# Optimization experiments

Hardware: AMD Instinct MI355X
Metric: run time of the kernel (lower is better)

## Reference

```python
import jax, jax.numpy as jnp
import numpy as np

B, S, D = 16, 2048, 128
NEG = -1000000000.0


def setup_inputs() -> dict:
    key = jax.random.key(0)
    kq, kk, kv = jax.random.split(key, 3)
    q = jax.random.normal(kq, (B, S, D), dtype=jnp.float32)
    k = jax.random.normal(kk, (B, S, D), dtype=jnp.float32)
    v = jax.random.normal(kv, (B, S, D), dtype=jnp.float32)
    # causal mask: True entries are masked out (filled with -1e9)
    mask = jnp.broadcast_to(
        jnp.triu(jnp.ones((S, S), dtype=bool), k=1)[None, :, :], (B, S, S)
    )
    return {"q": q, "k": k, "v": v, "mask": mask}


def reference(q, k, v, mask):
    # attn = q @ k^T / sqrt(d_k), masked_fill, softmax over keys, attn @ v
    scale = jnp.sqrt(jnp.asarray(D, dtype=q.dtype))
    attn = jnp.einsum("bqd,bkd->bqk", q, k) / scale
    attn = jnp.where(mask, jnp.asarray(NEG, dtype=attn.dtype), attn)
    attn = jax.nn.softmax(attn, axis=2)
    out = jnp.einsum("bqk,bkd->bqd", attn, v)
    return (out, attn)
```

## Files before the change

### kernel.cpp

```cpp
#include <hip/hip_runtime.h>

#define B_ 16
#define S_ 2048
#define D_ 128

typedef __attribute__((ext_vector_type(8))) short bf16x8;
typedef __attribute__((ext_vector_type(4))) float f32x4;
typedef __attribute__((ext_vector_type(16))) float f32x16;
typedef __attribute__((ext_vector_type(2))) unsigned int u32x2;
typedef __attribute__((ext_vector_type(4))) unsigned int u32x4;

__device__ __forceinline__ unsigned short f2bf(float f) {
    unsigned int u = __builtin_bit_cast(unsigned int, f);
    u += 0x7fff + ((u >> 16) & 1);
    return (unsigned short)(u >> 16);
}

__device__ __forceinline__ void gload16(const void* g, void* l) {
    __builtin_amdgcn_global_load_lds(
        (const __attribute__((address_space(1))) void*)g,
        (__attribute__((address_space(3))) void*)l, 16, 0, 0);
}

#define WAITV(n) asm volatile("s_waitcnt vmcnt(" #n ")" ::: "memory")

__global__ __launch_bounds__(256, 4)
void conv_kv(const float* __restrict__ kg, const float* __restrict__ vg,
             char* __restrict__ kws, char* __restrict__ vws)
{
    __shared__ float lt[64 * 132];
    const int bid = blockIdx.x;
    if (bid < 512) {
        const float* src = kg + ((long)bid << 13);
        char* dst = kws + ((long)bid << 14);
#pragma unroll
        for (int it = 0; it < 4; ++it) {
            const int c = threadIdx.x + it * 256;
            const int r = c >> 4, j = c & 15;
            f32x4 a = *(const f32x4*)(src + r * 128 + j * 8);
            f32x4 cc = *(const f32x4*)(src + r * 128 + j * 8 + 4);
            u32x4 p;
            p[0] = (unsigned)f2bf(a[0]) | ((unsigned)f2bf(a[1]) << 16);
            p[1] = (unsigned)f2bf(a[2]) | ((unsigned)f2bf(a[3]) << 16);
            p[2] = (unsigned)f2bf(cc[0]) | ((unsigned)f2bf(cc[1]) << 16);
            p[3] = (unsigned)f2bf(cc[2]) | ((unsigned)f2bf(cc[3]) << 16);
            *(u32x4*)(dst + r * 256 + ((j ^ (r & 7)) << 4)) = p;
        }
    } else {
        const int vb = bid - 512;
        const float* src = vg + ((long)vb << 13);
        char* dst = vws + ((long)vb << 14);
#pragma unroll
        for (int it = 0; it < 8; ++it) {
            const int c = threadIdx.x + it * 256;
            const int r = c >> 5, q = c & 31;
            *(f32x4*)(lt + r * 132 + q * 4) = *(const f32x4*)(src + r * 128 + q * 4);
        }
        __syncthreads();
#pragma unroll
        for (int it = 0; it < 4; ++it) {
            const int c = threadIdx.x + it * 256;
            const int d = c >> 3, jc = c & 7;
            unsigned short e[8];
#pragma unroll
            for (int ee = 0; ee < 8; ++ee) e[ee] = f2bf(lt[(jc * 8 + ee) * 132 + d]);
            u32x4 p;
            p[0] = (unsigned)e[0] | ((unsigned)e[1] << 16);
            p[1] = (unsigned)e[2] | ((unsigned)e[3] << 16);
            p[2] = (unsigned)e[4] | ((unsigned)e[5] << 16);
            p[3] = (unsigned)e[6] | ((unsigned)e[7] << 16);
            *(u32x4*)(dst + d * 128 + ((jc ^ (d & 7)) << 4)) = p;
        }
    }
}

__device__ __forceinline__ int qtile_of(int b, int t) {
    const int f = (t & 1) ? (t >> 1) : (31 - (t >> 1));
    return (b & 8) ? (31 - f) : f;
}

__global__ __launch_bounds__(256, 4)
void sumexp(const float* __restrict__ qg, const char* __restrict__ kws,
            float* __restrict__ lg, float* __restrict__ attng)
{
    __shared__ char kT[2][16384];

    const int tid = threadIdx.x, lane = tid & 63, w = tid >> 6;
    const int l15 = lane & 15, l4 = lane >> 4;
    const int bid = blockIdx.x;
    const int b = bid >> 5;
    const int qt = qtile_of(b, bid & 31);
    const int q0 = qt * 64;
    const float scale = 0.088388347648318447f;

    bf16x8 qf[4];
    {
        const float* qrow = qg + ((long)b * S_ + q0 + w * 16 + l15) * D_;
#pragma unroll
        for (int kk = 0; kk < 4; ++kk) {
            const int d0 = kk * 32 + l4 * 8;
            f32x4 a = *(const f32x4*)(qrow + d0);
            f32x4 c = *(const f32x4*)(qrow + d0 + 4);
            bf16x8 tt;
            tt[0] = (short)f2bf(a[0]); tt[1] = (short)f2bf(a[1]);
            tt[2] = (short)f2bf(a[2]); tt[3] = (short)f2bf(a[3]);
            tt[4] = (short)f2bf(c[0]); tt[5] = (short)f2bf(c[1]);
            tt[6] = (short)f2bf(c[2]); tt[7] = (short)f2bf(c[3]);
            qf[kk] = tt;
        }
    }
    WAITV(0);

    float sum[4] = {0.f, 0.f, 0.f, 0.f};
    const char* kb0 = kws + ((long)(b * 32) << 14);

#pragma unroll
    for (int it = 0; it < 4; ++it)
        gload16(kb0 + (w * 4 + it) * 1024 + lane * 16, &kT[0][(w * 4 + it) * 1024]);

    int buf = 0;
    for (int kt = 0; kt <= qt; ++kt) {
        const bool pf = (kt < qt);
        if (pf) {
            const char* kn = kb0 + ((long)(kt + 1) << 14);
#pragma unroll
            for (int it = 0; it < 4; ++it)
                gload16(kn + (w * 4 + it) * 1024 + lane * 16, &kT[buf ^ 1][(w * 4 + it) * 1024]);
            WAITV(4);
        } else {
            WAITV(0);
        }
        __builtin_amdgcn_s_barrier();
        __builtin_amdgcn_sched_barrier(0);

        f32x4 acc[4];
        __builtin_amdgcn_s_setprio(1);
#pragma unroll
        for (int n = 0; n < 4; ++n) {
            f32x4 a = {0.f, 0.f, 0.f, 0.f};
            const int krow = n * 16 + l15;
            const int rb = krow * 256;
            const int swz = (krow & 7) << 4;
#pragma unroll
            for (int kk = 0; kk < 4; ++kk) {
                bf16x8 bf = *(const bf16x8*)(&kT[buf][rb + ((l4 * 16 + kk * 64) ^ swz)]);
                a = __builtin_amdgcn_mfma_f32_16x16x32_bf16(qf[kk], bf, a, 0, 0, 0);
            }
            acc[n] = a;
        }
        __builtin_amdgcn_s_setprio(0);

        const bool diag = (kt == qt);
#pragma unroll
        for (int n = 0; n < 4; ++n)
#pragma unroll
            for (int r = 0; r < 4; ++r) {
                if (!(diag && (n * 16 + l15 > w * 16 + l4 * 4 + r)))
                    sum[r] += __expf(acc[n][r] * scale);
            }
        __builtin_amdgcn_sched_barrier(0);
        __builtin_amdgcn_s_barrier();
        buf ^= 1;
    }

#pragma unroll
    for (int off = 1; off < 16; off <<= 1)
#pragma unroll
        for (int r = 0; r < 4; ++r)
            sum[r] += __shfl_xor(sum[r], off, 64);
    if (l15 == 0) {
#pragma unroll
        for (int r = 0; r < 4; ++r)
            lg[(long)b * S_ + q0 + w * 16 + l4 * 4 + r] = 1.f / sum[r];
    }

    float* attn_base = attng + ((long)b * S_ + q0) * S_;
    const int col0 = (qt + 1) * 64;
    if (col0 < S_) {
        const int nch = (S_ - col0) >> 2;
        const f32x4 z = {0.f, 0.f, 0.f, 0.f};
        for (int row = w; row < 64; row += 4) {
            float* rbase = attn_base + (long)row * S_ + col0;
            for (int c = lane; c < nch; c += 64)
                *(f32x4*)(rbase + c * 4) = z;
        }
    }
}

__global__ __launch_bounds__(256, 2)
void attn_pv(const float* __restrict__ qg, const char* __restrict__ kws,
             const char* __restrict__ vws, const float* __restrict__ lg,
             float* __restrict__ outg, float* __restrict__ attng)
{
    __shared__ char lds[65536];

    const int tid = threadIdx.x, lane = tid & 63, w = tid >> 6;
    const int wq = w >> 1, wk = w & 1;
    const int l31 = lane & 31, hi = lane >> 5;
    const int bid = blockIdx.x;
    const int b = bid >> 5;
    const int qti = qtile_of(b, bid & 31);
    const int q0 = qti * 64;
    const int nt = qti + 1;
    const float scale = 0.088388347648318447f;
    const int qrow = q0 + wq * 32 + l31;

    bf16x8 qf[8];
    {
        const float* qr = qg + ((long)b * S_ + qrow) * D_;
#pragma unroll
        for (int km = 0; km < 8; ++km) {
            const int d0 = km * 16 + hi * 8;
            f32x4 a = *(const f32x4*)(qr + d0);
            f32x4 c = *(const f32x4*)(qr + d0 + 4);
            bf16x8 t;
            t[0] = (short)f2bf(a[0]); t[1] = (short)f2bf(a[1]);
            t[2] = (short)f2bf(a[2]); t[3] = (short)f2bf(a[3]);
            t[4] = (short)f2bf(c[0]); t[5] = (short)f2bf(c[1]);
            t[6] = (short)f2bf(c[2]); t[7] = (short)f2bf(c[3]);
            qf[km] = t;
        }
    }
    const float invl_l = lg[(long)b * S_ + qrow];
    WAITV(0);

    f32x16 oacc[4];
#pragma unroll
    for (int dt = 0; dt < 4; ++dt)
#pragma unroll
        for (int i = 0; i < 16; ++i) oacc[dt][i] = 0.f;

    const char* kb0 = kws + ((long)(b * 32) << 14);
    const char* vb0 = vws + ((long)(b * 32) << 14);

#pragma unroll
    for (int it = 0; it < 4; ++it)
        gload16(kb0 + it * 4096 + tid * 16, lds + it * 4096 + tid * 16);
#pragma unroll
    for (int it = 0; it < 4; ++it)
        gload16(vb0 + it * 4096 + tid * 16, lds + 32768 + it * 4096 + tid * 16);

    const int krow = wk * 32 + l31;
    const int krb = krow * 256;
    const int ksw = krow & 7;

    int buf = 0;
    for (int kt = 0; kt < nt; ++kt) {
        const bool pf = (kt + 1 < nt);
        if (pf) {
            const char* kn = kb0 + ((long)(kt + 1) << 14);
            const char* vn = vb0 + ((long)(kt + 1) << 14);
            const int db = (buf ^ 1) * 16384;
#pragma unroll
            for (int it = 0; it < 4; ++it)
                gload16(kn + it * 4096 + tid * 16, lds + db + it * 4096 + tid * 16);
#pragma unroll
            for (int it = 0; it < 4; ++it)
                gload16(vn + it * 4096 + tid * 16, lds + 32768 + db + it * 4096 + tid * 16);
        }
        if (kt == 0) { if (pf) { WAITV(8); } else { WAITV(0); } }
        else         { if (pf) { WAITV(12); } else { WAITV(4); } }
        __builtin_amdgcn_s_barrier();
        __builtin_amdgcn_sched_barrier(0);

        const char* kbuf = lds + buf * 16384;
        const char* vbuf = lds + 32768 + buf * 16384;

        f32x16 acc;
#pragma unroll
        for (int i = 0; i < 16; ++i) acc[i] = 0.f;
        __builtin_amdgcn_s_setprio(1);
#pragma unroll
        for (int km = 0; km < 8; ++km) {
            bf16x8 kf = *(const bf16x8*)(kbuf + krb + (((km * 2 + hi) ^ ksw) << 4));
            acc = __builtin_amdgcn_mfma_f32_32x32x16_bf16(kf, qf[km], acc, 0, 0, 0);
        }
        __builtin_amdgcn_s_setprio(0);

        const int kbase = kt * 64 + wk * 32;
        float p[16];
#pragma unroll
        for (int r = 0; r < 16; ++r) {
            const int kl = (r & 3) + 8 * (r >> 2) + 4 * hi;
            p[r] = (kbase + kl > qrow) ? 0.f : __expf(acc[r] * scale);
        }
        unsigned W[8], PW[8];
#pragma unroll
        for (int i = 0; i < 8; ++i)
            W[i] = (unsigned)f2bf(p[2 * i]) | ((unsigned)f2bf(p[2 * i + 1]) << 16);
#pragma unroll
        for (int i = 0; i < 8; ++i)
            PW[i] = (unsigned)__shfl_xor((int)W[i], 32, 64);

        bf16x8 pa[2];
        float* arow = attng + ((long)b * S_ + qrow) * S_ + kbase;
#pragma unroll
        for (int kc = 0; kc < 2; ++kc) {
            u32x4 fr;
            fr[0] = hi ? PW[kc * 4 + 2] : W[kc * 4 + 0];
            fr[1] = hi ? PW[kc * 4 + 3] : W[kc * 4 + 1];
            fr[2] = hi ? W[kc * 4 + 2] : PW[kc * 4 + 0];
            fr[3] = hi ? W[kc * 4 + 3] : PW[kc * 4 + 1];
            pa[kc] = __builtin_bit_cast(bf16x8, fr);
            f32x4 s0, s1;
            s0[0] = __builtin_bit_cast(float, fr[0] << 16) * invl_l;
            s0[1] = __builtin_bit_cast(float, fr[0] & 0xffff0000u) * invl_l;
            s0[2] = __builtin_bit_cast(float, fr[1] << 16) * invl_l;
            s0[3] = __builtin_bit_cast(float, fr[1] & 0xffff0000u) * invl_l;
            s1[0] = __builtin_bit_cast(float, fr[2] << 16) * invl_l;
            s1[1] = __builtin_bit_cast(float, fr[2] & 0xffff0000u) * invl_l;
            s1[2] = __builtin_bit_cast(float, fr[3] << 16) * invl_l;
            s1[3] = __builtin_bit_cast(float, fr[3] & 0xffff0000u) * invl_l;
            *(f32x4*)(arow + kc * 16 + hi * 8) = s0;
            *(f32x4*)(arow + kc * 16 + hi * 8 + 4) = s1;
        }

        __builtin_amdgcn_s_setprio(1);
#pragma unroll
        for (int dt = 0; dt < 4; ++dt) {
            const int d = dt * 32 + l31;
            const int rowb = d * 128;
            const int sw = (d & 7) << 4;
#pragma unroll
            for (int kc = 0; kc < 2; ++kc) {
                const int jc = wk * 4 + kc * 2 + hi;
                bf16x8 vf = *(const bf16x8*)(vbuf + rowb + ((jc << 4) ^ sw));
                oacc[dt] = __builtin_amdgcn_mfma_f32_32x32x16_bf16(pa[kc], vf, oacc[dt], 0, 0, 0);
            }
        }
        __builtin_amdgcn_s_setprio(0);
        __builtin_amdgcn_sched_barrier(0);
        __builtin_amdgcn_s_barrier();
        buf ^= 1;
    }

    __syncthreads();
    float* red = (float*)lds;
    if (wk) {
#pragma unroll
        for (int dt = 0; dt < 4; ++dt)
#pragma unroll
            for (int r = 0; r < 16; ++r) {
                const int qr = (r & 3) + 8 * (r >> 2) + 4 * hi;
                red[wq * 4096 + qr * 128 + dt * 32 + l31] = oacc[dt][r];
            }
    }
    __syncthreads();
    if (!wk) {
        float iv[16];
#pragma unroll
        for (int r = 0; r < 16; ++r) {
            const int qr = (r & 3) + 8 * (r >> 2) + 4 * hi;
            iv[r] = __shfl(invl_l, qr, 64);
        }
        float* ob = outg + ((long)b * S_ + q0 + wq * 32) * D_;
#pragma unroll
        for (int dt = 0; dt < 4; ++dt)
#pragma unroll
            for (int r = 0; r < 16; ++r) {
                const int qr = (r & 3) + 8 * (r >> 2) + 4 * hi;
                ob[(long)qr * D_ + dt * 32 + l31] =
                    (oacc[dt][r] + red[wq * 4096 + qr * 128 + dt * 32 + l31]) * iv[r];
            }
    }
}

__global__ __launch_bounds__(256, 2)
void attn_fallback(const float* __restrict__ qg, const float* __restrict__ kg,
                   const float* __restrict__ vg,
                   float* __restrict__ outg, float* __restrict__ attng)
{
    __shared__ unsigned short kT[64 * 128];
    __shared__ unsigned short vT[128 * 64];
    __shared__ unsigned short pT[4][16 * 64];
    const int tid = threadIdx.x, lane = tid & 63, w = tid >> 6;
    const int l15 = lane & 15, l4 = lane >> 4;
    const int bid = blockIdx.x;
    const int b = bid >> 5, qt = 31 - (bid & 31), q0 = qt * 64;
    const float scale = 0.088388347648318447f;
    bf16x8 qf[4];
    {
        const float* qrow = qg + ((long)b * S_ + q0 + w * 16 + l15) * D_;
#pragma unroll
        for (int kk = 0; kk < 4; ++kk) {
            const int d0 = kk * 32 + l4 * 8;
            f32x4 a = *(const f32x4*)(qrow + d0);
            f32x4 c = *(const f32x4*)(qrow + d0 + 4);
            bf16x8 t;
            t[0] = (short)f2bf(a[0]); t[1] = (short)f2bf(a[1]);
            t[2] = (short)f2bf(a[2]); t[3] = (short)f2bf(a[3]);
            t[4] = (short)f2bf(c[0]); t[5] = (short)f2bf(c[1]);
            t[6] = (short)f2bf(c[2]); t[7] = (short)f2bf(c[3]);
            qf[kk] = t;
        }
    }
    float m[4], l[4];
#pragma unroll
    for (int r = 0; r < 4; ++r) { m[r] = -1e30f; l[r] = 0.f; }
    for (int kt = 0; kt <= qt; ++kt) {
        __syncthreads();
        {
            const float* kbase = kg + ((long)b * S_ + kt * 64) * D_;
#pragma unroll
            for (int it = 0; it < 8; ++it) {
                const int c = tid + it * 256, row = c >> 5, dc = c & 31;
                f32x4 a = *(const f32x4*)(kbase + row * D_ + dc * 4);
                u32x2 p;
                p[0] = (unsigned)f2bf(a[0]) | ((unsigned)f2bf(a[1]) << 16);
                p[1] = (unsigned)f2bf(a[2]) | ((unsigned)f2bf(a[3]) << 16);
                *(u32x2*)((char*)kT + row * 256 + ((dc * 8) ^ ((row & 7) << 4))) = p;
            }
        }
        __syncthreads();
        f32x4 acc[4];
#pragma unroll
        for (int n = 0; n < 4; ++n) {
            f32x4 a = {0.f, 0.f, 0.f, 0.f};
            const int krow = n * 16 + l15, rb = krow * 256, swz = (krow & 7) << 4;
#pragma unroll
            for (int kk = 0; kk < 4; ++kk) {
                bf16x8 bf = *(const bf16x8*)((const char*)kT + rb + ((l4 * 16 + kk * 64) ^ swz));
                a = __builtin_amdgcn_mfma_f32_16x16x32_bf16(qf[kk], bf, a, 0, 0, 0);
            }
            acc[n] = a;
        }
        const bool diag = (kt == qt);
        float tm[4] = {-3e38f, -3e38f, -3e38f, -3e38f};
#pragma unroll
        for (int n = 0; n < 4; ++n)
#pragma unroll
            for (int r = 0; r < 4; ++r) {
                float s = acc[n][r] * scale;
                if (diag && (n * 16 + l15 > w * 16 + l4 * 4 + r)) s = -3e38f;
                acc[n][r] = s; tm[r] = fmaxf(tm[r], s);
            }
#pragma unroll
        for (int off = 1; off < 16; off <<= 1)
#pragma unroll
            for (int r = 0; r < 4; ++r) tm[r] = fmaxf(tm[r], __shfl_xor(tm[r], off, 64));
        float sum[4], mn[4];
#pragma unroll
        for (int r = 0; r < 4; ++r) {
            mn[r] = fmaxf(m[r], tm[r]);
            float s0 = 0.f;
#pragma unroll
            for (int n = 0; n < 4; ++n) s0 += __expf(acc[n][r] - mn[r]);
            sum[r] = s0;
        }
#pragma unroll
        for (int off = 1; off < 16; off <<= 1)
#pragma unroll
            for (int r = 0; r < 4; ++r) sum[r] += __shfl_xor(sum[r], off, 64);
#pragma unroll
        for (int r = 0; r < 4; ++r) { l[r] = l[r] * __expf(m[r] - mn[r]) + sum[r]; m[r] = mn[r]; }
    }
    float invl[4];
#pragma unroll
    for (int r = 0; r < 4; ++r) invl[r] = 1.f / l[r];
    f32x4 oacc[8];
#pragma unroll
    for (int n = 0; n < 8; ++n) oacc[n] = (f32x4){0.f, 0.f, 0.f, 0.f};
    float* attn_base = attng + ((long)b * S_ + q0) * S_;
    for (int kt = 0; kt <= qt; ++kt) {
        __syncthreads();
        {
            const float* kbase = kg + ((long)b * S_ + kt * 64) * D_;
#pragma unroll
            for (int it = 0; it < 8; ++it) {
                const int c = tid + it * 256, row = c >> 5, dc = c & 31;
                f32x4 a = *(const f32x4*)(kbase + row * D_ + dc * 4);
                u32x2 p;
                p[0] = (unsigned)f2bf(a[0]) | ((unsigned)f2bf(a[1]) << 16);
                p[1] = (unsigned)f2bf(a[2]) | ((unsigned)f2bf(a[3]) << 16);
                *(u32x2*)((char*)kT + row * 256 + ((dc * 8) ^ ((row & 7) << 4))) = p;
            }
        }
        {
            const float* vbase = vg + ((long)b * S_ + kt * 64) * D_;
#pragma unroll
            for (int it = 0; it < 8; ++it) {
                const int c = tid + it * 256, kr = c & 63, dq = c >> 6;
                f32x4 a = *(const f32x4*)(vbase + kr * D_ + dq * 4);
#pragma unroll
                for (int j = 0; j < 4; ++j) {
                    const int d = dq * 4 + j;
                    *(unsigned short*)((char*)vT + d * 128 + ((kr * 2) ^ ((d & 7) << 4))) = f2bf(a[j]);
                }
            }
        }
        __syncthreads();
        f32x4 acc[4];
#pragma unroll
        for (int n = 0; n < 4; ++n) {
            f32x4 a = {0.f, 0.f, 0.f, 0.f};
            const int krow = n * 16 + l15, rb = krow * 256, swz = (krow & 7) << 4;
#pragma unroll
            for (int kk = 0; kk < 4; ++kk) {
                bf16x8 bf = *(const bf16x8*)((const char*)kT + rb + ((l4 * 16 + kk * 64) ^ swz));
                a = __builtin_amdgcn_mfma_f32_16x16x32_bf16(qf[kk], bf, a, 0, 0, 0);
            }
            acc[n] = a;
        }
        const bool diag = (kt == qt);
#pragma unroll
        for (int n = 0; n < 4; ++n)
#pragma unroll
            for (int r = 0; r < 4; ++r) {
                float s = acc[n][r] * scale;
                if (diag && (n * 16 + l15 > w * 16 + l4 * 4 + r)) s = -3e38f;
                const float p = __expf(s - m[r]) * invl[r];
                attn_base[(long)(w * 16 + l4 * 4 + r) * S_ + kt * 64 + n * 16 + l15] = p;
                const int prow = l4 * 4 + r;
                *(unsigned short*)((char*)&pT[w][0] + prow * 128 + ((n * 32 + l15 * 2) ^ ((prow & 7) << 4))) = f2bf(p);
            }
        asm volatile("s_waitcnt lgkmcnt(0)" ::: "memory");
        __builtin_amdgcn_sched_barrier(0);
        bf16x8 pa[2];
#pragma unroll
        for (int kk = 0; kk < 2; ++kk)
            pa[kk] = *(const bf16x8*)((const char*)&pT[w][0] + l15 * 128 + ((l4 * 16 + kk * 64) ^ ((l15 & 7) << 4)));
#pragma unroll
        for (int n = 0; n < 8; ++n) {
            const int vrow = n * 16 + l15, rb = vrow * 128, swz = (vrow & 7) << 4;
#pragma unroll
            for (int kk = 0; kk < 2; ++kk) {
                bf16x8 bv = *(const bf16x8*)((const char*)vT + rb + ((l4 * 16 + kk * 64) ^ swz));
                oacc[n] = __builtin_amdgcn_mfma_f32_16x16x32_bf16(pa[kk], bv, oacc[n], 0, 0, 0);
            }
        }
    }
    {
        float* obase = outg + ((long)b * S_ + q0 + w * 16) * D_;
#pragma unroll
        for (int n = 0; n < 8; ++n)
#pragma unroll
            for (int r = 0; r < 4; ++r)
                obase[(long)(l4 * 4 + r) * D_ + n * 16 + l15] = oacc[n][r];
    }
    {
        const int col0 = (qt + 1) * 64;
        if (col0 < S_) {
            const int nch = (S_ - col0) >> 2;
            const f32x4 z = {0.f, 0.f, 0.f, 0.f};
            for (int row = w; row < 64; row += 4) {
                float* rbase = attn_base + (long)row * S_ + col0;
                for (int c = lane; c < nch; c += 64)
                    *(f32x4*)(rbase + c * 4) = z;
            }
        }
    }
}

extern "C" void kernel_launch(void* const* d_in, const int* in_sizes, int n_in,
                              void* d_out, int out_size, void* d_ws, size_t ws_size,
                              hipStream_t stream) {
    const float* q = (const float*)d_in[0];
    const float* k = (const float*)d_in[1];
    const float* v = (const float*)d_in[2];
    float* out  = (float*)d_out;
    float* attn = out + (long)B_ * S_ * D_;
    const size_t NEED = 131072 + 2u * 8388608u;
    if (ws_size >= NEED) {
        float* lg = (float*)d_ws;
        char* kws = (char*)d_ws + 131072;
        char* vws = kws + 8388608;
        conv_kv<<<dim3(1024), dim3(256), 0, stream>>>(k, v, kws, vws);
        sumexp<<<dim3(512), dim3(256), 0, stream>>>(q, kws, lg, attn);
        attn_pv<<<dim3(512), dim3(256), 0, stream>>>(q, kws, vws, lg, out, attn);
    } else {
        attn_fallback<<<dim3(512), dim3(256), 0, stream>>>(q, k, v, out, attn);
    }
}
```

Measured before the change: 120.3 us.

## Pre-layout K/V in MFMA fragment order and load directly to registers

The conversion kernel now writes bf16 K and V into a layout that matches the per-lane MFMA operand order, so sumexp and attn_pv read fragments straight from global memory into registers instead of staging through LDS with async copies and barriers. Work is reassigned per block as two 32-row query strips paired from opposite ends (strip u and 63-u) for causal load balance, with the two key halves split across waves and reduced through a small shared buffer. Register prefetch of the next K/V tile replaces LDS double buffering. This removes LDS traffic and barrier synchronisation but relies on L2 for reuse and raises register pressure.

After: 139.9 us. +16.3%, slower.

```diff
diff --git a/kernel.cpp b/kernel.cpp
--- a/kernel.cpp
+++ b/kernel.cpp
@@ -15,14 +15,6 @@
     u += 0x7fff + ((u >> 16) & 1);
     return (unsigned short)(u >> 16);
 }
-
-__device__ __forceinline__ void gload16(const void* g, void* l) {
-    __builtin_amdgcn_global_load_lds(
-        (const __attribute__((address_space(1))) void*)g,
-        (__attribute__((address_space(3))) void*)l, 16, 0, 0);
-}
-
-#define WAITV(n) asm volatile("s_waitcnt vmcnt(" #n ")" ::: "memory")
 
 __global__ __launch_bounds__(256, 4)
 void conv_kv(const float* __restrict__ kg, const float* __restrict__ vg,
@@ -44,7 +36,8 @@
             p[1] = (unsigned)f2bf(a[2]) | ((unsigned)f2bf(a[3]) << 16);
             p[2] = (unsigned)f2bf(cc[0]) | ((unsigned)f2bf(cc[1]) << 16);
             p[3] = (unsigned)f2bf(cc[2]) | ((unsigned)f2bf(cc[3]) << 16);
-            *(u32x4*)(dst + r * 256 + ((j ^ (r & 7)) << 4)) = p;
+            const int h = r >> 5, l31 = r & 31, km = j >> 1, hi = j & 1;
+            *(u32x4*)(dst + h * 8192 + km * 1024 + (hi * 32 + l31) * 16) = p;
         }
     } else {
         const int vb = bid - 512;
@@ -69,120 +62,92 @@
             p[1] = (unsigned)e[2] | ((unsigned)e[3] << 16);
             p[2] = (unsigned)e[4] | ((unsigned)e[5] << 16);
             p[3] = (unsigned)e[6] | ((unsigned)e[7] << 16);
-            *(u32x4*)(dst + d * 128 + ((jc ^ (d & 7)) << 4)) = p;
+            const int h = jc >> 2, kc = (jc >> 1) & 1, hi = jc & 1;
+            const int dt = d >> 5, l31 = d & 31;
+            *(u32x4*)(dst + h * 8192 + dt * 2048 + kc * 1024 + (hi * 32 + l31) * 16) = p;
         }
     }
 }
 
-__device__ __forceinline__ int qtile_of(int b, int t) {
-    const int f = (t & 1) ? (t >> 1) : (31 - (t >> 1));
-    return (b & 8) ? (31 - f) : f;
-}
 
 __global__ __launch_bounds__(256, 4)
 void sumexp(const float* __restrict__ qg, const char* __restrict__ kws,
             float* __restrict__ lg, float* __restrict__ attng)
 {
-    __shared__ char kT[2][16384];
-
+    __shared__ float redsum[2][2][32];
     const int tid = threadIdx.x, lane = tid & 63, w = tid >> 6;
-    const int l15 = lane & 15, l4 = lane >> 4;
+    const int l31 = lane & 31, hi = lane >> 5;
     const int bid = blockIdx.x;
-    const int b = bid >> 5;
-    const int qt = qtile_of(b, bid & 31);
-    const int q0 = qt * 64;
+    const int b = bid >> 5, u = bid & 31;
+    const int sidx = w >> 1, kh = w & 1;
+    const int strip = sidx ? u : (63 - u);
+    const int q0 = strip * 32;
+    const int qrow = q0 + l31;
+    const int nst = strip + 1;
     const float scale = 0.088388347648318447f;
 
-    bf16x8 qf[4];
+    bf16x8 qf[8];
     {
-        const float* qrow = qg + ((long)b * S_ + q0 + w * 16 + l15) * D_;
-#pragma unroll
-        for (int kk = 0; kk < 4; ++kk) {
-            const int d0 = kk * 32 + l4 * 8;
-            f32x4 a = *(const f32x4*)(qrow + d0);
-            f32x4 c = *(const f32x4*)(qrow + d0 + 4);
+        const float* qr = qg + ((long)b * S_ + qrow) * D_;
+#pragma unroll
+        for (int km = 0; km < 8; ++km) {
+            const int d0 = km * 16 + hi * 8;
+            f32x4 a = *(const f32x4*)(qr + d0);
+            f32x4 c = *(const f32x4*)(qr + d0 + 4);
             bf16x8 tt;
             tt[0] = (short)f2bf(a[0]); tt[1] = (short)f2bf(a[1]);
             tt[2] = (short)f2bf(a[2]); tt[3] = (short)f2bf(a[3]);
             tt[4] = (short)f2bf(c[0]); tt[5] = (short)f2bf(c[1]);
             tt[6] = (short)f2bf(c[2]); tt[7] = (short)f2bf(c[3]);
-            qf[kk] = tt;
-        }
-    }
-    WAITV(0);
-
-    float sum[4] = {0.f, 0.f, 0.f, 0.f};
+            qf[km] = tt;
+        }
+    }
+
     const char* kb0 = kws + ((long)(b * 32) << 14);
-
-#pragma unroll
-    for (int it = 0; it < 4; ++it)
-        gload16(kb0 + (w * 4 + it) * 1024 + lane * 16, &kT[0][(w * 4 + it) * 1024]);
-
-    int buf = 0;
-    for (int kt = 0; kt <= qt; ++kt) {
-        const bool pf = (kt < qt);
-        if (pf) {
-            const char* kn = kb0 + ((long)(kt + 1) << 14);
-#pragma unroll
-            for (int it = 0; it < 4; ++it)
-                gload16(kn + (w * 4 + it) * 1024 + lane * 16, &kT[buf ^ 1][(w * 4 + it) * 1024]);
-            WAITV(4);
-        } else {
-            WAITV(0);
-        }
-        __builtin_amdgcn_s_barrier();
-        __builtin_amdgcn_sched_barrier(0);
-
-        f32x4 acc[4];
-        __builtin_amdgcn_s_setprio(1);
-#pragma unroll
-        for (int n = 0; n < 4; ++n) {
-            f32x4 a = {0.f, 0.f, 0.f, 0.f};
-            const int krow = n * 16 + l15;
-            const int rb = krow * 256;
-            const int swz = (krow & 7) << 4;
-#pragma unroll
-            for (int kk = 0; kk < 4; ++kk) {
-                bf16x8 bf = *(const bf16x8*)(&kT[buf][rb + ((l4 * 16 + kk * 64) ^ swz)]);
-                a = __builtin_amdgcn_mfma_f32_16x16x32_bf16(qf[kk], bf, a, 0, 0, 0);
-            }
-            acc[n] = a;
-        }
-        __builtin_amdgcn_s_setprio(0);
-
-        const bool diag = (kt == qt);
-#pragma unroll
-        for (int n = 0; n < 4; ++n)
-#pragma unroll
-            for (int r = 0; r < 4; ++r) {
-                if (!(diag && (n * 16 + l15 > w * 16 + l4 * 4 + r)))
-                    sum[r] += __expf(acc[n][r] * scale);
-            }
-        __builtin_amdgcn_sched_barrier(0);
-        __builtin_amdgcn_s_barrier();
-        buf ^= 1;
-    }
-
-#pragma unroll
-    for (int off = 1; off < 16; off <<= 1)
-#pragma unroll
-        for (int r = 0; r < 4; ++r)
-            sum[r] += __shfl_xor(sum[r], off, 64);
-    if (l15 == 0) {
-#pragma unroll
-        for (int r = 0; r < 4; ++r)
-            lg[(long)b * S_ + q0 + w * 16 + l4 * 4 + r] = 1.f / sum[r];
-    }
-
-    float* attn_base = attng + ((long)b * S_ + q0) * S_;
-    const int col0 = (qt + 1) * 64;
+    float sum = 0.f;
+    if (kh < nst) {
+        bf16x8 kf[8];
+#pragma unroll
+        for (int km = 0; km < 8; ++km)
+            kf[km] = *(const bf16x8*)(kb0 + kh * 8192 + km * 1024 + lane * 16);
+        for (int j = kh; j < nst; j += 2) {
+            f32x16 acc;
+#pragma unroll
+            for (int i = 0; i < 16; ++i) acc[i] = 0.f;
+            __builtin_amdgcn_s_setprio(1);
+#pragma unroll
+            for (int km = 0; km < 8; ++km)
+                acc = __builtin_amdgcn_mfma_f32_32x32x16_bf16(kf[km], qf[km], acc, 0, 0, 0);
+            __builtin_amdgcn_s_setprio(0);
+            if (j + 2 < nst) {
+                const char* kn = kb0 + ((j + 2) >> 1) * 16384 + ((j + 2) & 1) * 8192;
+#pragma unroll
+                for (int km = 0; km < 8; ++km)
+                    kf[km] = *(const bf16x8*)(kn + km * 1024 + lane * 16);
+            }
+            const int kbase = j * 32;
+#pragma unroll
+            for (int r = 0; r < 16; ++r) {
+                const int kl = (r & 3) + 8 * (r >> 2) + 4 * hi;
+                if (kbase + kl <= qrow) sum += __expf(acc[r] * scale);
+            }
+        }
+    }
+    sum += __shfl_xor(sum, 32, 64);
+    redsum[sidx][kh][l31] = sum;
+    __syncthreads();
+    if (kh == 0 && !hi)
+        lg[(long)b * S_ + qrow] = 1.f / (sum + redsum[sidx][1][l31]);
+
+    const int col0 = ((strip >> 1) + 1) * 64;
     if (col0 < S_) {
         const int nch = (S_ - col0) >> 2;
         const f32x4 z = {0.f, 0.f, 0.f, 0.f};
-        for (int row = w; row < 64; row += 4) {
-            float* rbase = attn_base + (long)row * S_ + col0;
+        float* base = attng + ((long)b * S_ + q0 + kh * 16) * S_ + col0;
+        for (int row = 0; row < 16; ++row) {
+            float* rb = base + (long)row * S_;
             for (int c = lane; c < nch; c += 64)
-                *(f32x4*)(rbase + c * 4) = z;
+                *(f32x4*)(rb + c * 4) = z;
         }
     }
 }
@@ -192,18 +157,17 @@
              const char* __restrict__ vws, const float* __restrict__ lg,
              float* __restrict__ outg, float* __restrict__ attng)
 {
-    __shared__ char lds[65536];
-
+    __shared__ float red[2][32][128];
     const int tid = threadIdx.x, lane = tid & 63, w = tid >> 6;
-    const int wq = w >> 1, wk = w & 1;
     const int l31 = lane & 31, hi = lane >> 5;
     const int bid = blockIdx.x;
-    const int b = bid >> 5;
-    const int qti = qtile_of(b, bid & 31);
-    const int q0 = qti * 64;
-    const int nt = qti + 1;
+    const int b = bid >> 5, u = bid & 31;
+    const int sidx = w >> 1, kh = w & 1;
+    const int strip = sidx ? u : (63 - u);
+    const int q0 = strip * 32;
+    const int qrow = q0 + l31;
+    const int nst = (strip | 1) + 1;
     const float scale = 0.088388347648318447f;
-    const int qrow = q0 + wq * 32 + l31;
 
     bf16x8 qf[8];
     {
@@ -213,16 +177,15 @@
             const int d0 = km * 16 + hi * 8;
             f32x4 a = *(const f32x4*)(qr + d0);
             f32x4 c = *(const f32x4*)(qr + d0 + 4);
-            bf16x8 t;
-            t[0] = (short)f2bf(a[0]); t[1] = (short)f2bf(a[1]);
-            t[2] = (short)f2bf(a[2]); t[3] = (short)f2bf(a[3]);
-            t[4] = (short)f2bf(c[0]); t[5] = (short)f2bf(c[1]);
-            t[6] = (short)f2bf(c[2]); t[7] = (short)f2bf(c[3]);
-            qf[km] = t;
+            bf16x8 tt;
+            tt[0] = (short)f2bf(a[0]); tt[1] = (short)f2bf(a[1]);
+            tt[2] = (short)f2bf(a[2]); tt[3] = (short)f2bf(a[3]);
+            tt[4] = (short)f2bf(c[0]); tt[5] = (short)f2bf(c[1]);
+            tt[6] = (short)f2bf(c[2]); tt[7] = (short)f2bf(c[3]);
+            qf[km] = tt;
         }
     }
     const float invl_l = lg[(long)b * S_ + qrow];
-    WAITV(0);
 
     f32x16 oacc[4];
 #pragma unroll
@@ -232,68 +195,49 @@
 
     const char* kb0 = kws + ((long)(b * 32) << 14);
     const char* vb0 = vws + ((long)(b * 32) << 14);
-
-#pragma unroll
-    for (int it = 0; it < 4; ++it)
-        gload16(kb0 + it * 4096 + tid * 16, lds + it * 4096 + tid * 16);
-#pragma unroll
-    for (int it = 0; it < 4; ++it)
-        gload16(vb0 + it * 4096 + tid * 16, lds + 32768 + it * 4096 + tid * 16);
-
-    const int krow = wk * 32 + l31;
-    const int krb = krow * 256;
-    const int ksw = krow & 7;
-
-    int buf = 0;
-    for (int kt = 0; kt < nt; ++kt) {
-        const bool pf = (kt + 1 < nt);
-        if (pf) {
-            const char* kn = kb0 + ((long)(kt + 1) << 14);
-            const char* vn = vb0 + ((long)(kt + 1) << 14);
-            const int db = (buf ^ 1) * 16384;
-#pragma unroll
-            for (int it = 0; it < 4; ++it)
-                gload16(kn + it * 4096 + tid * 16, lds + db + it * 4096 + tid * 16);
-#pragma unroll
-            for (int it = 0; it < 4; ++it)
-                gload16(vn + it * 4096 + tid * 16, lds + 32768 + db + it * 4096 + tid * 16);
-        }
-        if (kt == 0) { if (pf) { WAITV(8); } else { WAITV(0); } }
-        else         { if (pf) { WAITV(12); } else { WAITV(4); } }
-        __builtin_amdgcn_s_barrier();
-        __builtin_amdgcn_sched_barrier(0);
-
-        const char* kbuf = lds + buf * 16384;
-        const char* vbuf = lds + 32768 + buf * 16384;
-
+    float* attn_row = attng + ((long)b * S_ + qrow) * S_;
+
+    bf16x8 kf[8], vf[8];
+#pragma unroll
+    for (int km = 0; km < 8; ++km)
+        kf[km] = *(const bf16x8*)(kb0 + kh * 8192 + km * 1024 + lane * 16);
+#pragma unroll
+    for (int f = 0; f < 8; ++f)
+        vf[f] = *(const bf16x8*)(vb0 + kh * 8192 + f * 1024 + lane * 16);
+
+    for (int j = kh; j < nst; j += 2) {
         f32x16 acc;
 #pragma unroll
         for (int i = 0; i < 16; ++i) acc[i] = 0.f;
         __builtin_amdgcn_s_setprio(1);
 #pragma unroll
-        for (int km = 0; km < 8; ++km) {
-            bf16x8 kf = *(const bf16x8*)(kbuf + krb + (((km * 2 + hi) ^ ksw) << 4));
-            acc = __builtin_amdgcn_mfma_f32_32x32x16_bf16(kf, qf[km], acc, 0, 0, 0);
-        }
+        for (int km = 0; km < 8; ++km)
+            acc = __builtin_amdgcn_mfma_f32_32x32x16_bf16(kf[km], qf[km], acc, 0, 0, 0);
         __builtin_amdgcn_s_setprio(0);
 
-        const int kbase = kt * 64 + wk * 32;
-        float p[16];
-#pragma unroll
-        for (int r = 0; r < 16; ++r) {
-            const int kl = (r & 3) + 8 * (r >> 2) + 4 * hi;
-            p[r] = (kbase + kl > qrow) ? 0.f : __expf(acc[r] * scale);
-        }
+        if (j + 2 < nst) {
+            const char* kn = kb0 + ((j + 2) >> 1) * 16384 + ((j + 2) & 1) * 8192;
+#pragma unroll
+            for (int km = 0; km < 8; ++km)
+                kf[km] = *(const bf16x8*)(kn + km * 1024 + lane * 16);
+        }
+
+        const int kbase = j * 32;
         unsigned W[8], PW[8];
 #pragma unroll
-        for (int i = 0; i < 8; ++i)
-            W[i] = (unsigned)f2bf(p[2 * i]) | ((unsigned)f2bf(p[2 * i + 1]) << 16);
+        for (int i = 0; i < 8; ++i) {
+            const int r0 = 2 * i;
+            const int kl0 = (r0 & 3) + 8 * (r0 >> 2) + 4 * hi;
+            const float p0 = (kbase + kl0 > qrow) ? 0.f : __expf(acc[r0] * scale);
+            const float p1 = (kbase + kl0 + 1 > qrow) ? 0.f : __expf(acc[r0 + 1] * scale);
+            W[i] = (unsigned)f2bf(p0) | ((unsigned)f2bf(p1) << 16);
+        }
 #pragma unroll
         for (int i = 0; i < 8; ++i)
             PW[i] = (unsigned)__shfl_xor((int)W[i], 32, 64);
 
         bf16x8 pa[2];
-        float* arow = attng + ((long)b * S_ + qrow) * S_ + kbase;
+        float* arow = attn_row + kbase;
 #pragma unroll
         for (int kc = 0; kc < 2; ++kc) {
             u32x4 fr;
@@ -317,50 +261,45 @@
 
         __builtin_amdgcn_s_setprio(1);
 #pragma unroll
-        for (int dt = 0; dt < 4; ++dt) {
-            const int d = dt * 32 + l31;
-            const int rowb = d * 128;
-            const int sw = (d & 7) << 4;
-#pragma unroll
-            for (int kc = 0; kc < 2; ++kc) {
-                const int jc = wk * 4 + kc * 2 + hi;
-                bf16x8 vf = *(const bf16x8*)(vbuf + rowb + ((jc << 4) ^ sw));
-                oacc[dt] = __builtin_amdgcn_mfma_f32_32x32x16_bf16(pa[kc], vf, oacc[dt], 0, 0, 0);
-            }
-        }
+        for (int dt = 0; dt < 4; ++dt)
+#pragma unroll
+            for (int kc = 0; kc < 2; ++kc)
+                oacc[dt] = __builtin_amdgcn_mfma_f32_32x32x16_bf16(pa[kc], vf[dt * 2 + kc], oacc[dt], 0, 0, 0);
         __builtin_amdgcn_s_setprio(0);
-        __builtin_amdgcn_sched_barrier(0);
-        __builtin_amdgcn_s_barrier();
-        buf ^= 1;
-    }
-
-    __syncthreads();
-    float* red = (float*)lds;
-    if (wk) {
+
+        if (j + 2 < nst) {
+            const char* vn = vb0 + ((j + 2) >> 1) * 16384 + ((j + 2) & 1) * 8192;
+#pragma unroll
+            for (int f = 0; f < 8; ++f)
+                vf[f] = *(const bf16x8*)(vn + f * 1024 + lane * 16);
+        }
+    }
+
+    if (kh == 1) {
 #pragma unroll
         for (int dt = 0; dt < 4; ++dt)
 #pragma unroll
             for (int r = 0; r < 16; ++r) {
                 const int qr = (r & 3) + 8 * (r >> 2) + 4 * hi;
-                red[wq * 4096 + qr * 128 + dt * 32 + l31] = oacc[dt][r];
+                red[sidx][qr][dt * 32 + l31] = oacc[dt][r];
             }
     }
     __syncthreads();
-    if (!wk) {
+    if (kh == 0) {
         float iv[16];
 #pragma unroll
         for (int r = 0; r < 16; ++r) {
             const int qr = (r & 3) + 8 * (r >> 2) + 4 * hi;
             iv[r] = __shfl(invl_l, qr, 64);
         }
-        float* ob = outg + ((long)b * S_ + q0 + wq * 32) * D_;
+        float* ob = outg + ((long)b * S_ + q0) * D_;
 #pragma unroll
         for (int dt = 0; dt < 4; ++dt)
 #pragma unroll
             for (int r = 0; r < 16; ++r) {
                 const int qr = (r & 3) + 8 * (r >> 2) + 4 * hi;
                 ob[(long)qr * D_ + dt * 32 + l31] =
-                    (oacc[dt][r] + red[wq * 4096 + qr * 128 + dt * 32 + l31]) * iv[r];
+                    (oacc[dt][r] + red[sidx][qr][dt * 32 + l31]) * iv[r];
             }
     }
 }
```

## Fuse row-sum pass into attention kernel and move mask zero-fill to conversion kernel

Applied to the files above, without the earlier changes.

Drops the separate sumexp kernel and computes each row's softmax denominator inside the main attention kernel, using a first pass over K tiles before the P·V pass. The inverse sums go through LDS instead of a global workspace array. Zeroing the masked upper-triangle of attn moves into the K conversion blocks, with each block covering a complementary pair of tiles to balance the work. This saves a kernel launch and the global round-trip for the row sums, but the first pass now runs at 2 waves/CU occupancy instead of 4.

Result: no change. 122.3 us (+1.7%).

```diff
diff --git a/kernel.cpp b/kernel.cpp
--- a/kernel.cpp
+++ b/kernel.cpp
@@ -26,16 +26,18 @@
 
 __global__ __launch_bounds__(256, 4)
 void conv_kv(const float* __restrict__ kg, const float* __restrict__ vg,
-             char* __restrict__ kws, char* __restrict__ vws)
+             char* __restrict__ kws, char* __restrict__ vws, float* __restrict__ attng)
 {
     __shared__ float lt[64 * 132];
     const int bid = blockIdx.x;
+    const int tid = threadIdx.x;
     if (bid < 512) {
+        const int b = bid >> 5, t = bid & 31;
         const float* src = kg + ((long)bid << 13);
         char* dst = kws + ((long)bid << 14);
 #pragma unroll
         for (int it = 0; it < 4; ++it) {
-            const int c = threadIdx.x + it * 256;
+            const int c = tid + it * 256;
             const int r = c >> 4, j = c & 15;
             f32x4 a = *(const f32x4*)(src + r * 128 + j * 8);
             f32x4 cc = *(const f32x4*)(src + r * 128 + j * 8 + 4);
@@ -46,20 +48,40 @@
             p[3] = (unsigned)f2bf(cc[2]) | ((unsigned)f2bf(cc[3]) << 16);
             *(u32x4*)(dst + r * 256 + ((j ^ (r & 7)) << 4)) = p;
         }
+        const f32x4 z = {0.f, 0.f, 0.f, 0.f};
+        {
+            const int W4 = (31 - t) * 16;
+            float* base = attng + ((long)(b * S_) + t * 64) * S_ + (t + 1) * 64;
+            for (int row = 0; row < 32; ++row) {
+                float* rb = base + (long)row * S_;
+                for (int c = tid; c < W4; c += 256)
+                    *(f32x4*)(rb + c * 4) = z;
+            }
+        }
+        {
+            const int s = 31 - t;
+            const int W4 = t * 16;
+            float* base = attng + ((long)(b * S_) + s * 64 + 32) * S_ + (s + 1) * 64;
+            for (int row = 0; row < 32; ++row) {
+                float* rb = base + (long)row * S_;
+                for (int c = tid; c < W4; c += 256)
+                    *(f32x4*)(rb + c * 4) = z;
+            }
+        }
     } else {
         const int vb = bid - 512;
         const float* src = vg + ((long)vb << 13);
         char* dst = vws + ((long)vb << 14);
 #pragma unroll
         for (int it = 0; it < 8; ++it) {
-            const int c = threadIdx.x + it * 256;
+            const int c = tid + it * 256;
             const int r = c >> 5, q = c & 31;
             *(f32x4*)(lt + r * 132 + q * 4) = *(const f32x4*)(src + r * 128 + q * 4);
         }
         __syncthreads();
 #pragma unroll
         for (int it = 0; it < 4; ++it) {
-            const int c = threadIdx.x + it * 256;
+            const int c = tid + it * 256;
             const int d = c >> 3, jc = c & 7;
             unsigned short e[8];
 #pragma unroll
@@ -79,118 +101,10 @@
     return (b & 8) ? (31 - f) : f;
 }
 
-__global__ __launch_bounds__(256, 4)
-void sumexp(const float* __restrict__ qg, const char* __restrict__ kws,
-            float* __restrict__ lg, float* __restrict__ attng)
-{
-    __shared__ char kT[2][16384];
-
-    const int tid = threadIdx.x, lane = tid & 63, w = tid >> 6;
-    const int l15 = lane & 15, l4 = lane >> 4;
-    const int bid = blockIdx.x;
-    const int b = bid >> 5;
-    const int qt = qtile_of(b, bid & 31);
-    const int q0 = qt * 64;
-    const float scale = 0.088388347648318447f;
-
-    bf16x8 qf[4];
-    {
-        const float* qrow = qg + ((long)b * S_ + q0 + w * 16 + l15) * D_;
-#pragma unroll
-        for (int kk = 0; kk < 4; ++kk) {
-            const int d0 = kk * 32 + l4 * 8;
-            f32x4 a = *(const f32x4*)(qrow + d0);
-            f32x4 c = *(const f32x4*)(qrow + d0 + 4);
-            bf16x8 tt;
-            tt[0] = (short)f2bf(a[0]); tt[1] = (short)f2bf(a[1]);
-            tt[2] = (short)f2bf(a[2]); tt[3] = (short)f2bf(a[3]);
-            tt[4] = (short)f2bf(c[0]); tt[5] = (short)f2bf(c[1]);
-            tt[6] = (short)f2bf(c[2]); tt[7] = (short)f2bf(c[3]);
-            qf[kk] = tt;
-        }
-    }
-    WAITV(0);
-
-    float sum[4] = {0.f, 0.f, 0.f, 0.f};
-    const char* kb0 = kws + ((long)(b * 32) << 14);
-
-#pragma unroll
-    for (int it = 0; it < 4; ++it)
-        gload16(kb0 + (w * 4 + it) * 1024 + lane * 16, &kT[0][(w * 4 + it) * 1024]);
-
-    int buf = 0;
-    for (int kt = 0; kt <= qt; ++kt) {
-        const bool pf = (kt < qt);
-        if (pf) {
-            const char* kn = kb0 + ((long)(kt + 1) << 14);
-#pragma unroll
-            for (int it = 0; it < 4; ++it)
-                gload16(kn + (w * 4 + it) * 1024 + lane * 16, &kT[buf ^ 1][(w * 4 + it) * 1024]);
-            WAITV(4);
-        } else {
-            WAITV(0);
-        }
-        __builtin_amdgcn_s_barrier();
-        __builtin_amdgcn_sched_barrier(0);
-
-        f32x4 acc[4];
-        __builtin_amdgcn_s_setprio(1);
-#pragma unroll
-        for (int n = 0; n < 4; ++n) {
-            f32x4 a = {0.f, 0.f, 0.f, 0.f};
-            const int krow = n * 16 + l15;
-            const int rb = krow * 256;
-            const int swz = (krow & 7) << 4;
-#pragma unroll
-            for (int kk = 0; kk < 4; ++kk) {
-                bf16x8 bf = *(const bf16x8*)(&kT[buf][rb + ((l4 * 16 + kk * 64) ^ swz)]);
-                a = __builtin_amdgcn_mfma_f32_16x16x32_bf16(qf[kk], bf, a, 0, 0, 0);
-            }
-            acc[n] = a;
-        }
-        __builtin_amdgcn_s_setprio(0);
-
-        const bool diag = (kt == qt);
-#pragma unroll
-        for (int n = 0; n < 4; ++n)
-#pragma unroll
-            for (int r = 0; r < 4; ++r) {
-                if (!(diag && (n * 16 + l15 > w * 16 + l4 * 4 + r)))
-                    sum[r] += __expf(acc[n][r] * scale);
-            }
-        __builtin_amdgcn_sched_barrier(0);
-        __builtin_amdgcn_s_barrier();
-        buf ^= 1;
-    }
-
-#pragma unroll
-    for (int off = 1; off < 16; off <<= 1)
-#pragma unroll
-        for (int r = 0; r < 4; ++r)
-            sum[r] += __shfl_xor(sum[r], off, 64);
-    if (l15 == 0) {
-#pragma unroll
-        for (int r = 0; r < 4; ++r)
-            lg[(long)b * S_ + q0 + w * 16 + l4 * 4 + r] = 1.f / sum[r];
-    }
-
-    float* attn_base = attng + ((long)b * S_ + q0) * S_;
-    const int col0 = (qt + 1) * 64;
-    if (col0 < S_) {
-        const int nch = (S_ - col0) >> 2;
-        const f32x4 z = {0.f, 0.f, 0.f, 0.f};
-        for (int row = w; row < 64; row += 4) {
-            float* rbase = attn_base + (long)row * S_ + col0;
-            for (int c = lane; c < nch; c += 64)
-                *(f32x4*)(rbase + c * 4) = z;
-        }
-    }
-}
-
 __global__ __launch_bounds__(256, 2)
-void attn_pv(const float* __restrict__ qg, const char* __restrict__ kws,
-             const char* __restrict__ vws, const float* __restrict__ lg,
-             float* __restrict__ outg, float* __restrict__ attng)
+void flash_fused(const float* __restrict__ qg, const char* __restrict__ kws,
+                 const char* __restrict__ vws,
+                 float* __restrict__ outg, float* __restrict__ attng)
 {
     __shared__ char lds[65536];
 
@@ -199,9 +113,9 @@
     const int l31 = lane & 31, hi = lane >> 5;
     const int bid = blockIdx.x;
     const int b = bid >> 5;
-    const int qti = qtile_of(b, bid & 31);
-    const int q0 = qti * 64;
-    const int nt = qti + 1;
+    const int qt = qtile_of(b, bid & 31);
+    const int q0 = qt * 64;
+    const int nt = qt + 1;
     const float scale = 0.088388347648318447f;
     const int qrow = q0 + wq * 32 + l31;
 
@@ -221,30 +135,82 @@
             qf[km] = t;
         }
     }
-    const float invl_l = lg[(long)b * S_ + qrow];
     WAITV(0);
-
-    f32x16 oacc[4];
-#pragma unroll
-    for (int dt = 0; dt < 4; ++dt)
-#pragma unroll
-        for (int i = 0; i < 16; ++i) oacc[dt][i] = 0.f;
 
     const char* kb0 = kws + ((long)(b * 32) << 14);
     const char* vb0 = vws + ((long)(b * 32) << 14);
-
-#pragma unroll
-    for (int it = 0; it < 4; ++it)
-        gload16(kb0 + it * 4096 + tid * 16, lds + it * 4096 + tid * 16);
-#pragma unroll
-    for (int it = 0; it < 4; ++it)
-        gload16(vb0 + it * 4096 + tid * 16, lds + 32768 + it * 4096 + tid * 16);
 
     const int krow = wk * 32 + l31;
     const int krb = krow * 256;
     const int ksw = krow & 7;
 
+#pragma unroll
+    for (int it = 0; it < 4; ++it)
+        gload16(kb0 + it * 4096 + tid * 16, lds + it * 4096 + tid * 16);
+
+    float sumA = 0.f;
     int buf = 0;
+    for (int kt = 0; kt < nt; ++kt) {
+        const bool pf = (kt + 1 < nt);
+        if (pf) {
+            const char* kn = kb0 + ((long)(kt + 1) << 14);
+            const int db = (buf ^ 1) * 16384;
+#pragma unroll
+            for (int it = 0; it < 4; ++it)
+                gload16(kn + it * 4096 + tid * 16, lds + db + it * 4096 + tid * 16);
+            WAITV(4);
+        } else {
+            WAITV(0);
+        }
+        __builtin_amdgcn_s_barrier();
+        __builtin_amdgcn_sched_barrier(0);
+
+        const char* kbuf = lds + buf * 16384;
+        f32x16 acc;
+#pragma unroll
+        for (int i = 0; i < 16; ++i) acc[i] = 0.f;
+        __builtin_amdgcn_s_setprio(1);
+#pragma unroll
+        for (int km = 0; km < 8; ++km) {
+            bf16x8 kf = *(const bf16x8*)(kbuf + krb + (((km * 2 + hi) ^ ksw) << 4));
+            acc = __builtin_amdgcn_mfma_f32_32x32x16_bf16(kf, qf[km], acc, 0, 0, 0);
+        }
+        __builtin_amdgcn_s_setprio(0);
+
+        const int kbase = kt * 64 + wk * 32;
+#pragma unroll
+        for (int r = 0; r < 16; ++r) {
+            const int kl = (r & 3) + 8 * (r >> 2) + 4 * hi;
+            if (kbase + kl <= qrow) sumA += __expf(acc[r] * scale);
+        }
+        __builtin_amdgcn_sched_barrier(0);
+        __builtin_amdgcn_s_barrier();
+        buf ^= 1;
+    }
+
+    sumA += __shfl_xor(sumA, 32, 64);
+    float* sums = (float*)lds;
+    if (!hi) sums[(wq * 2 + wk) * 32 + l31] = sumA;
+    __syncthreads();
+    const float invl_l = 1.f / (sums[(wq * 2 + 0) * 32 + l31] + sums[(wq * 2 + 1) * 32 + l31]);
+    __syncthreads();
+
+    f32x16 oacc[4];
+#pragma unroll
+    for (int dt = 0; dt < 4; ++dt)
+#pragma unroll
+        for (int i = 0; i < 16; ++i) oacc[dt][i] = 0.f;
+
+    float* attn_row = attng + ((long)b * S_ + qrow) * S_;
+
+#pragma unroll
+    for (int it = 0; it < 4; ++it)
+        gload16(kb0 + it * 4096 + tid * 16, lds + it * 4096 + tid * 16);
+#pragma unroll
+    for (int it = 0; it < 4; ++it)
+        gload16(vb0 + it * 4096 + tid * 16, lds + 32768 + it * 4096 + tid * 16);
+
+    buf = 0;
     for (int kt = 0; kt < nt; ++kt) {
         const bool pf = (kt + 1 < nt);
         if (pf) {
@@ -278,22 +244,21 @@
         __builtin_amdgcn_s_setprio(0);
 
         const int kbase = kt * 64 + wk * 32;
-        float p[16];
-#pragma unroll
-        for (int r = 0; r < 16; ++r) {
-            const int kl = (r & 3) + 8 * (r >> 2) + 4 * hi;
-            p[r] = (kbase + kl > qrow) ? 0.f : __expf(acc[r] * scale);
-        }
         unsigned W[8], PW[8];
 #pragma unroll
-        for (int i = 0; i < 8; ++i)
-            W[i] = (unsigned)f2bf(p[2 * i]) | ((unsigned)f2bf(p[2 * i + 1]) << 16);
+        for (int i = 0; i < 8; ++i) {
+            const int r0 = 2 * i;
+            const int kl0 = (r0 & 3) + 8 * (r0 >> 2) + 4 * hi;
+            const float p0 = (kbase + kl0 > qrow) ? 0.f : __expf(acc[r0] * scale);
+            const float p1 = (kbase + kl0 + 1 > qrow) ? 0.f : __expf(acc[r0 + 1] * scale);
+            W[i] = (unsigned)f2bf(p0) | ((unsigned)f2bf(p1) << 16);
+        }
 #pragma unroll
         for (int i = 0; i < 8; ++i)
             PW[i] = (unsigned)__shfl_xor((int)W[i], 32, 64);
 
         bf16x8 pa[2];
-        float* arow = attng + ((long)b * S_ + qrow) * S_ + kbase;
+        float* arow = attn_row + kbase;
 #pragma unroll
         for (int kc = 0; kc < 2; ++kc) {
             u32x4 fr;
@@ -559,14 +524,12 @@
     const float* v = (const float*)d_in[2];
     float* out  = (float*)d_out;
     float* attn = out + (long)B_ * S_ * D_;
-    const size_t NEED = 131072 + 2u * 8388608u;
+    const size_t NEED = 2u * 8388608u;
     if (ws_size >= NEED) {
-        float* lg = (float*)d_ws;
-        char* kws = (char*)d_ws + 131072;
+        char* kws = (char*)d_ws;
         char* vws = kws + 8388608;
-        conv_kv<<<dim3(1024), dim3(256), 0, stream>>>(k, v, kws, vws);
-        sumexp<<<dim3(512), dim3(256), 0, stream>>>(q, kws, lg, attn);
-        attn_pv<<<dim3(512), dim3(256), 0, stream>>>(q, kws, vws, lg, out, attn);
+        conv_kv<<<dim3(1024), dim3(256), 0, stream>>>(k, v, kws, vws, attn);
+        flash_fused<<<dim3(512), dim3(256), 0, stream>>>(q, kws, vws, out, attn);
     } else {
         attn_fallback<<<dim3(512), dim3(256), 0, stream>>>(q, k, v, out, attn);
     }
```
